# Performance work log

Measured on AMD Instinct MI355X. Metric: run time of the kernel, lower is better.

## Reference

```python
import jax, jax.numpy as jnp
import numpy as np

B, CIN, C, H, W = 8, 256, 128, 128, 128
BN_EPS = 1e-5
EPS = 1e-12


def _bn_params(k, c):
    k1, k2, k3, k4 = jax.random.split(k, 4)
    gamma = jax.random.uniform(k1, (c,), minval=0.5, maxval=1.5)
    beta = jax.random.normal(k2, (c,)) * 0.1
    mean = jax.random.normal(k3, (c,)) * 0.1
    var = jax.random.uniform(k4, (c,), minval=0.5, maxval=1.5)
    return gamma, beta, mean, var


def _xavier(k, cout, cin):
    lim = np.sqrt(6.0 / (cin + cout))
    return jax.random.uniform(k, (cout, cin), minval=-lim, maxval=lim)


def setup_inputs() -> dict:
    key = jax.random.key(0)
    ks = jax.random.split(key, 16)
    inp = {
        'target_task_feats': jax.random.normal(ks[0], (B, CIN, H, W), dtype=jnp.float32),
        'source_task_feats': jax.random.normal(ks[1], (B, CIN, H, W), dtype=jnp.float32),
        'q_w1': _xavier(ks[2], C, CIN), 'q_w2': _xavier(ks[3], C, C),
        'k_w1': _xavier(ks[4], C, CIN), 'k_w2': _xavier(ks[5], C, C),
        'v_w': _xavier(ks[6], C, CIN),
    }
    for name, kk, c in [('q1', ks[7], C), ('q2', ks[8], C), ('k1', ks[9], C), ('k2', ks[10], C), ('v', ks[11], C)]:
        g, b, m, v = _bn_params(kk, c)
        inp[f'{name}_g'], inp[f'{name}_b'], inp[f'{name}_m'], inp[f'{name}_v'] = g, b, m, v
    return inp


def _conv_bn(x, w, g, b, m, v):
    # 1x1 conv (no bias) + eval-mode BatchNorm, fused scale/shift
    y = jnp.einsum('bchw,oc->bohw', x, w)
    scale = (g / jnp.sqrt(v + BN_EPS))[None, :, None, None]
    shift = (b - m * g / jnp.sqrt(v + BN_EPS))[None, :, None, None]
    return y * scale + shift


def reference(target_task_feats, source_task_feats,
              q_w1, q_w2, k_w1, k_w2, v_w,
              q1_g, q1_b, q1_m, q1_v,
              q2_g, q2_b, q2_m, q2_v,
              k1_g, k1_b, k1_m, k1_v,
              k2_g, k2_b, k2_m, k2_v,
              v_g, v_b, v_m, v_v):
    b = target_task_feats.shape[0]
    # key / value from source
    k_h = jax.nn.relu(_conv_bn(source_task_feats, k_w1, k1_g, k1_b, k1_m, k1_v))
    key = jax.nn.softplus(_conv_bn(k_h, k_w2, k2_g, k2_b, k2_m, k2_v)).reshape(b, C, -1)  # [B,C,Ns]
    value = jax.nn.relu(_conv_bn(source_task_feats, v_w, v_g, v_b, v_m, v_v)).reshape(b, C, -1)  # [B,C,Ns]
    # query from target
    q_h = jax.nn.relu(_conv_bn(target_task_feats, q_w1, q1_g, q1_b, q1_m, q1_v))
    query = jax.nn.softplus(_conv_bn(q_h, q_w2, q2_g, q2_b, q2_m, q2_v)).reshape(b, C, -1)  # [B,C,Nt]
    # linear attention: KV^T then Q
    S = jnp.einsum('bcn,bdn->bcd', value, key)      # [B,C,C]
    Z = key.sum(axis=2)                              # [B,C]
    denom = jnp.einsum('bc,bcn->bn', Z, query)[:, None, :]  # [B,1,Nt]
    out = jnp.einsum('bcd,bdn->bcn', S, query) / jnp.maximum(denom, EPS)
    return out.reshape(b, C, H, W)
```

## Files before the change

### kernel.cpp

```cpp
#include <hip/hip_runtime.h>
#include <math.h>

typedef __attribute__((ext_vector_type(8))) short bf8v;
typedef __attribute__((ext_vector_type(4))) float f4v;

#define B_      8
#define CIN_    256
#define C_      128
#define NPIX_   16384
#define EPS_    1e-12f
#define BN_EPS_ 1e-5f

#define OFF_WK1  0u
#define OFF_WV   65536u
#define OFF_WQ1  131072u
#define OFF_WK2  196608u
#define OFF_WQ2  229376u
#define OFF_BIAS 262144u
#define OFF_S    264704u
#define OFF_Z    788992u
#define OFF_SBF  793088u
#define OFF_VAL  1055232u
#define OFF_KEY  34609664u

__device__ __forceinline__ unsigned short f2bf(float f) {
    unsigned u = __float_as_uint(f);
    unsigned r = u + 0x7fffu + ((u >> 16) & 1u);
    return (unsigned short)(r >> 16);
}
__device__ __forceinline__ float lo16(unsigned v){ return __uint_as_float(v << 16); }
__device__ __forceinline__ float hi16(unsigned v){ return __uint_as_float(v & 0xffff0000u); }
__device__ __forceinline__ float softplus_f(float x) {
    return fmaxf(x, 0.f) + __logf(1.f + __expf(-fabsf(x)));
}
__device__ __forceinline__ f4v MFMA(bf8v a, bf8v b, f4v c) {
    return __builtin_amdgcn_mfma_f32_16x16x32_bf16(a, b, c, 0, 0, 0);
}

struct PrepPtrs {
    const float* w[5];
    const float* g[5];
    const float* be[5];
    const float* mu[5];
    const float* va[5];
    unsigned short* wout[5];
    float* bout[5];
};

__global__ void prep_kernel(PrepPtrs p) {
    int idx = blockIdx.x * 256 + threadIdx.x;
    if (idx < 131072) {
        int conv, local, sh;
        if (idx < 32768)       { conv = 0; local = idx;          sh = 8; }
        else if (idx < 65536)  { conv = 1; local = idx - 32768;  sh = 8; }
        else if (idx < 98304)  { conv = 2; local = idx - 65536;  sh = 8; }
        else if (idx < 114688) { conv = 3; local = idx - 98304;  sh = 7; }
        else                   { conv = 4; local = idx - 114688; sh = 7; }
        int o = local >> sh;
        float scale = p.g[conv][o] * rsqrtf(p.va[conv][o] + BN_EPS_);
        p.wout[conv][local] = f2bf(p.w[conv][local] * scale);
    } else if (idx < 131712) {
        int j = idx - 131072;
        int conv = j >> 7;
        int o = j & 127;
        float scale = p.g[conv][o] * rsqrtf(p.va[conv][o] + BN_EPS_);
        p.bout[conv][o] = p.be[conv][o] - p.mu[conv][o] * scale;
    }
}

__global__ __launch_bounds__(256)
void srcKV(const float* __restrict__ src,
           const unsigned short* __restrict__ Wk1, const unsigned short* __restrict__ Wv,
           const unsigned short* __restrict__ Wk2, const float* __restrict__ bias,
           unsigned short* __restrict__ valg, unsigned short* __restrict__ keyg)
{
    __shared__ __align__(16) char smem[52224];
    unsigned short* xT = (unsigned short*)smem;
    unsigned short* hT = (unsigned short*)(smem + 33792);

    const int tid = threadIdx.x;
    const int L = tid & 63, w = tid >> 6;
    const int lr = L & 15, qd = L >> 4;
    const int b = blockIdx.y;
    const int gn0 = blockIdx.x * 64;
    const int m0 = w * 32;
    const int kbq = qd * 8;
    const float* bk1 = bias + 0;
    const float* bvp = bias + 128;
    const float* bk2 = bias + 384;

    #pragma unroll
    for (int s = 0; s < 4; s++) {
        int id = tid + s * 256;
        int n4 = (id & 15) * 4;
        int k0 = (id >> 4) * 4;
        float4 r[4];
        #pragma unroll
        for (int i = 0; i < 4; i++)
            r[i] = *(const float4*)(src + (size_t)(b * 256 + k0 + i) * NPIX_ + gn0 + n4);
        #pragma unroll
        for (int j = 0; j < 4; j++) {
            ushort4 t;
            t.x = f2bf(((const float*)&r[0])[j]);
            t.y = f2bf(((const float*)&r[1])[j]);
            t.z = f2bf(((const float*)&r[2])[j]);
            t.w = f2bf(((const float*)&r[3])[j]);
            *(ushort4*)(xT + (n4 + j) * 264 + k0) = t;
        }
    }
    __syncthreads();

    f4v zz = {0.f, 0.f, 0.f, 0.f};
    f4v hAcc[2][4], vAcc[2][4];
    #pragma unroll
    for (int mt = 0; mt < 2; mt++)
        #pragma unroll
        for (int nt = 0; nt < 4; nt++) { hAcc[mt][nt] = zz; vAcc[mt][nt] = zz; }
    #pragma unroll
    for (int ks = 0; ks < 8; ks++) {
        const int kb = ks * 32 + kbq;
        bf8v a1[2], a2[2], bx[4];
        #pragma unroll
        for (int mt = 0; mt < 2; mt++) {
            a1[mt] = *(const bf8v*)(Wk1 + (m0 + mt * 16 + lr) * 256 + kb);
            a2[mt] = *(const bf8v*)(Wv  + (m0 + mt * 16 + lr) * 256 + kb);
        }
        #pragma unroll
        for (int nt = 0; nt < 4; nt++)
            bx[nt] = *(const bf8v*)(xT + (nt * 16 + lr) * 264 + kb);
        #pragma unroll
        for (int mt = 0; mt < 2; mt++)
            #pragma unroll
            for (int nt = 0; nt < 4; nt++) {
                hAcc[mt][nt] = MFMA(a1[mt], bx[nt], hAcc[mt][nt]);
                vAcc[mt][nt] = MFMA(a2[mt], bx[nt], vAcc[mt][nt]);
            }
    }
    #pragma unroll
    for (int mt = 0; mt < 2; mt++) {
        const float4 b4 = *(const float4*)(bk1 + m0 + mt * 16 + qd * 4);
        #pragma unroll
        for (int nt = 0; nt < 4; nt++) {
            ushort4 t;
            t.x = f2bf(fmaxf(hAcc[mt][nt][0] + b4.x, 0.f));
            t.y = f2bf(fmaxf(hAcc[mt][nt][1] + b4.y, 0.f));
            t.z = f2bf(fmaxf(hAcc[mt][nt][2] + b4.z, 0.f));
            t.w = f2bf(fmaxf(hAcc[mt][nt][3] + b4.w, 0.f));
            *(ushort4*)(hT + (nt * 16 + lr) * 136 + m0 + mt * 16 + qd * 4) = t;
        }
    }
    __syncthreads();
    #pragma unroll
    for (int mt = 0; mt < 2; mt++) {
        const float4 b4 = *(const float4*)(bvp + m0 + mt * 16 + qd * 4);
        const float* bp = (const float*)&b4;
        #pragma unroll
        for (int nt = 0; nt < 4; nt++)
            #pragma unroll
            for (int r = 0; r < 4; r++)
                vAcc[mt][nt][r] = fmaxf(vAcc[mt][nt][r] + bp[r], 0.f);
    }

    f4v kAcc[2][4];
    #pragma unroll
    for (int mt = 0; mt < 2; mt++)
        #pragma unroll
        for (int nt = 0; nt < 4; nt++) kAcc[mt][nt] = zz;
    #pragma unroll
    for (int ks = 0; ks < 4; ks++) {
        const int kb = ks * 32 + kbq;
        bf8v a[2], bh[4];
        #pragma unroll
        for (int mt = 0; mt < 2; mt++)
            a[mt] = *(const bf8v*)(Wk2 + (m0 + mt * 16 + lr) * 128 + kb);
        #pragma unroll
        for (int nt = 0; nt < 4; nt++)
            bh[nt] = *(const bf8v*)(hT + (nt * 16 + lr) * 136 + kb);
        #pragma unroll
        for (int mt = 0; mt < 2; mt++)
            #pragma unroll
            for (int nt = 0; nt < 4; nt++)
                kAcc[mt][nt] = MFMA(a[mt], bh[nt], kAcc[mt][nt]);
    }
    __syncthreads();

    unsigned short* stgV = xT;
    unsigned short* stgK = hT;
    #pragma unroll
    for (int mt = 0; mt < 2; mt++) {
        const float4 b4 = *(const float4*)(bk2 + m0 + mt * 16 + qd * 4);
        const float* bp = (const float*)&b4;
        #pragma unroll
        for (int nt = 0; nt < 4; nt++)
            #pragma unroll
            for (int r = 0; r < 4; r++) {
                int m = m0 + mt * 16 + qd * 4 + r;
                stgV[m * 72 + nt * 16 + lr] = f2bf(vAcc[mt][nt][r]);
                stgK[m * 72 + nt * 16 + lr] = f2bf(softplus_f(kAcc[mt][nt][r] + bp[r]));
            }
    }
    __syncthreads();
    #pragma unroll
    for (int s = 0; s < 8; s++) {
        int id = tid + s * 256;
        int arr = id >> 10, rem = id & 1023;
        int c = rem >> 3, o = rem & 7;
        const unsigned short* sp = (arr ? stgK : stgV) + c * 72 + o * 8;
        uint4 d = *(const uint4*)sp;
        unsigned short* gp = (arr ? keyg : valg) + (size_t)(b * 128 + c) * NPIX_ + gn0 + o * 8;
        *(uint4*)gp = d;
    }
}

__global__ __launch_bounds__(256)
void skern(const unsigned short* __restrict__ valg, const unsigned short* __restrict__ keyg,
           float* __restrict__ Sbuf, float* __restrict__ Zbuf)
{
    __shared__ __align__(16) unsigned short vs[128 * 72];
    __shared__ __align__(16) unsigned short ks_[128 * 72];
    const int tid = threadIdx.x;
    const int L = tid & 63, w = tid >> 6;
    const int lr = L & 15, qd = L >> 4;
    const int b = blockIdx.x >> 5, ch = blockIdx.x & 31;
    const size_t nbase = (size_t)ch * 512;
    const int m0 = (w & 1) * 64, n0 = (w >> 1) * 64;

    f4v zz = {0.f, 0.f, 0.f, 0.f};
    f4v acc[4][4];
    #pragma unroll
    for (int mt = 0; mt < 4; mt++)
        #pragma unroll
        for (int nt = 0; nt < 4; nt++) acc[mt][nt] = zz;
    float zacc = 0.f;
    const int zc = tid >> 1, zh = tid & 1;

    for (int wd = 0; wd < 8; wd++) {
        const size_t nw = nbase + wd * 64;
        #pragma unroll
        for (int s = 0; s < 8; s++) {
            int id = tid + s * 256;
            int arr = id >> 10, rem = id & 1023;
            int c = rem >> 3, o = rem & 7;
            const unsigned short* g = (arr ? keyg : valg) + (size_t)(b * 128 + c) * NPIX_ + nw + o * 8;
            uint4 d = *(const uint4*)g;
            *(uint4*)((arr ? ks_ : vs) + c * 72 + o * 8) = d;
        }
        __syncthreads();
        #pragma unroll
        for (int kk = 0; kk < 2; kk++) {
            const int kb = kk * 32 + qd * 8;
            bf8v a[4], bb[4];
            #pragma unroll
            for (int mt = 0; mt < 4; mt++)
                a[mt] = *(const bf8v*)(vs + (m0 + mt * 16 + lr) * 72 + kb);
            #pragma unroll
            for (int nt = 0; nt < 4; nt++)
                bb[nt] = *(const bf8v*)(ks_ + (n0 + nt * 16 + lr) * 72 + kb);
            #pragma unroll
            for (int mt = 0; mt < 4; mt++)
                #pragma unroll
                for (int nt = 0; nt < 4; nt++)
                    acc[mt][nt] = MFMA(a[mt], bb[nt], acc[mt][nt]);
        }
        {
            const unsigned short* kr = ks_ + zc * 72 + zh * 32;
            #pragma unroll
            for (int p = 0; p < 4; p++) {
                uint4 t = *(const uint4*)(kr + p * 8);
                zacc += lo16(t.x) + hi16(t.x) + lo16(t.y) + hi16(t.y)
                      + lo16(t.z) + hi16(t.z) + lo16(t.w) + hi16(t.w);
            }
        }
        __syncthreads();
    }
    #pragma unroll
    for (int mt = 0; mt < 4; mt++)
        #pragma unroll
        for (int nt = 0; nt < 4; nt++)
            #pragma unroll
            for (int r = 0; r < 4; r++) {
                int m = m0 + mt * 16 + qd * 4 + r;
                int cN = n0 + nt * 16 + lr;
                atomicAdd(Sbuf + ((size_t)b * 128 + m) * 128 + cN, acc[mt][nt][r]);
            }
    atomicAdd(Zbuf + b * 128 + zc, zacc);
}

__global__ void cvts(const float* __restrict__ Sbuf, unsigned short* __restrict__ Sbf) {
    int i = blockIdx.x * 256 + threadIdx.x;
    if (i < 131072) Sbf[i] = f2bf(Sbuf[i]);
}

__global__ __launch_bounds__(256)
void tgtAttn(const float* __restrict__ tgt,
             const unsigned short* __restrict__ Wq1, const unsigned short* __restrict__ Wq2,
             const float* __restrict__ bias, const unsigned short* __restrict__ Sbf,
             const float* __restrict__ Zbuf, float* __restrict__ out)
{
    __shared__ __align__(16) char smem[51968];
    unsigned short* xT = (unsigned short*)smem;
    unsigned short* qT = (unsigned short*)(smem + 33792);
    float* dn  = (float*)(smem + 33792 + 17408);
    float* Zsh = dn + 64;

    const int tid = threadIdx.x;
    const int L = tid & 63, w = tid >> 6;
    const int lr = L & 15, qd = L >> 4;
    const int b = blockIdx.y;
    const int gn0 = blockIdx.x * 64;
    const int m0 = w * 32;
    const int kbq = qd * 8;
    const float* bq1 = bias + 256;
    const float* bq2 = bias + 512;

    if (tid < 128) Zsh[tid] = Zbuf[b * 128 + tid];
    #pragma unroll
    for (int s = 0; s < 4; s++) {
        int id = tid + s * 256;
        int n4 = (id & 15) * 4;
        int k0 = (id >> 4) * 4;
        float4 r[4];
        #pragma unroll
        for (int i = 0; i < 4; i++)
            r[i] = *(const float4*)(tgt + (size_t)(b * 256 + k0 + i) * NPIX_ + gn0 + n4);
        #pragma unroll
        for (int j = 0; j < 4; j++) {
            ushort4 t;
            t.x = f2bf(((const float*)&r[0])[j]);
            t.y = f2bf(((const float*)&r[1])[j]);
            t.z = f2bf(((const float*)&r[2])[j]);
            t.w = f2bf(((const float*)&r[3])[j]);
            *(ushort4*)(xT + (n4 + j) * 264 + k0) = t;
        }
    }
    __syncthreads();

    f4v zz = {0.f, 0.f, 0.f, 0.f};
    f4v acc1[2][4];
    #pragma unroll
    for (int mt = 0; mt < 2; mt++)
        #pragma unroll
        for (int nt = 0; nt < 4; nt++) acc1[mt][nt] = zz;
    #pragma unroll
    for (int ks = 0; ks < 8; ks++) {
        const int kb = ks * 32 + kbq;
        bf8v a[2], bx[4];
        #pragma unroll
        for (int mt = 0; mt < 2; mt++)
            a[mt] = *(const bf8v*)(Wq1 + (m0 + mt * 16 + lr) * 256 + kb);
        #pragma unroll
        for (int nt = 0; nt < 4; nt++)
            bx[nt] = *(const bf8v*)(xT + (nt * 16 + lr) * 264 + kb);
        #pragma unroll
        for (int mt = 0; mt < 2; mt++)
            #pragma unroll
            for (int nt = 0; nt < 4; nt++)
                acc1[mt][nt] = MFMA(a[mt], bx[nt], acc1[mt][nt]);
    }
    #pragma unroll
    for (int mt = 0; mt < 2; mt++) {
        const float4 b4 = *(const float4*)(bq1 + m0 + mt * 16 + qd * 4);
        #pragma unroll
        for (int nt = 0; nt < 4; nt++) {
            ushort4 t;
            t.x = f2bf(fmaxf(acc1[mt][nt][0] + b4.x, 0.f));
            t.y = f2bf(fmaxf(acc1[mt][nt][1] + b4.y, 0.f));
            t.z = f2bf(fmaxf(acc1[mt][nt][2] + b4.z, 0.f));
            t.w = f2bf(fmaxf(acc1[mt][nt][3] + b4.w, 0.f));
            *(ushort4*)(qT + (nt * 16 + lr) * 136 + m0 + mt * 16 + qd * 4) = t;
        }
    }
    __syncthreads();

    f4v acc2[2][4];
    #pragma unroll
    for (int mt = 0; mt < 2; mt++)
        #pragma unroll
        for (int nt = 0; nt < 4; nt++) acc2[mt][nt] = zz;
    #pragma unroll
    for (int ks = 0; ks < 4; ks++) {
        const int kb = ks * 32 + kbq;
        bf8v a[2], bh[4];
        #pragma unroll
        for (int mt = 0; mt < 2; mt++)
            a[mt] = *(const bf8v*)(Wq2 + (m0 + mt * 16 + lr) * 128 + kb);
        #pragma unroll
        for (int nt = 0; nt < 4; nt++)
            bh[nt] = *(const bf8v*)(qT + (nt * 16 + lr) * 136 + kb);
        #pragma unroll
        for (int mt = 0; mt < 2; mt++)
            #pragma unroll
            for (int nt = 0; nt < 4; nt++)
                acc2[mt][nt] = MFMA(a[mt], bh[nt], acc2[mt][nt]);
    }
    __syncthreads();
    #pragma unroll
    for (int mt = 0; mt < 2; mt++) {
        const float4 b4 = *(const float4*)(bq2 + m0 + mt * 16 + qd * 4);
        const float* bp = (const float*)&b4;
        #pragma unroll
        for (int nt = 0; nt < 4; nt++) {
            ushort4 t;
            t.x = f2bf(softplus_f(acc2[mt][nt][0] + bp[0]));
            t.y = f2bf(softplus_f(acc2[mt][nt][1] + bp[1]));
            t.z = f2bf(softplus_f(acc2[mt][nt][2] + bp[2]));
            t.w = f2bf(softplus_f(acc2[mt][nt][3] + bp[3]));
            *(ushort4*)(qT + (nt * 16 + lr) * 136 + m0 + mt * 16 + qd * 4) = t;
        }
    }
    __syncthreads();

    if (tid < 64) {
        const unsigned short* qr = qT + tid * 136;
        float s = 0.f;
        #pragma unroll
        for (int d = 0; d < 128; d += 8) {
            uint4 t = *(const uint4*)(qr + d);
            s = fmaf(Zsh[d + 0], lo16(t.x), s);
            s = fmaf(Zsh[d + 1], hi16(t.x), s);
            s = fmaf(Zsh[d + 2], lo16(t.y), s);
            s = fmaf(Zsh[d + 3], hi16(t.y), s);
            s = fmaf(Zsh[d + 4], lo16(t.z), s);
            s = fmaf(Zsh[d + 5], hi16(t.z), s);
            s = fmaf(Zsh[d + 6], lo16(t.w), s);
            s = fmaf(Zsh[d + 7], hi16(t.w), s);
        }
        dn[tid] = fmaxf(s, EPS_);
    }

    f4v oacc[2][4];
    #pragma unroll
    for (int mt = 0; mt < 2; mt++)
        #pragma unroll
        for (int nt = 0; nt < 4; nt++) oacc[mt][nt] = zz;
    #pragma unroll
    for (int ks = 0; ks < 4; ks++) {
        const int kb = ks * 32 + kbq;
        bf8v a[2], bq[4];
        #pragma unroll
        for (int mt = 0; mt < 2; mt++)
            a[mt] = *(const bf8v*)(Sbf + (size_t)b * 16384 + (m0 + mt * 16 + lr) * 128 + kb);
        #pragma unroll
        for (int nt = 0; nt < 4; nt++)
            bq[nt] = *(const bf8v*)(qT + (nt * 16 + lr) * 136 + kb);
        #pragma unroll
        for (int mt = 0; mt < 2; mt++)
            #pragma unroll
            for (int nt = 0; nt < 4; nt++)
                oacc[mt][nt] = MFMA(a[mt], bq[nt], oacc[mt][nt]);
    }
    __syncthreads();

    float inv[4];
    #pragma unroll
    for (int nt = 0; nt < 4; nt++) inv[nt] = 1.f / dn[nt * 16 + lr];
    #pragma unroll
    for (int mt = 0; mt < 2; mt++)
        #pragma unroll
        for (int nt = 0; nt < 4; nt++)
            #pragma unroll
            for (int r = 0; r < 4; r++) {
                int m = m0 + mt * 16 + qd * 4 + r;
                out[(size_t)(b * 128 + m) * NPIX_ + gn0 + nt * 16 + lr] = oacc[mt][nt][r] * inv[nt];
            }
}

extern "C" void kernel_launch(void* const* d_in, const int* in_sizes, int n_in,
                              void* d_out, int out_size, void* d_ws, size_t ws_size,
                              hipStream_t stream)
{
    const float* tgt = (const float*)d_in[0];
    const float* src = (const float*)d_in[1];
    char* ws = (char*)d_ws;
    unsigned short* Wk1 = (unsigned short*)(ws + OFF_WK1);
    unsigned short* Wv  = (unsigned short*)(ws + OFF_WV);
    unsigned short* Wq1 = (unsigned short*)(ws + OFF_WQ1);
    unsigned short* Wk2 = (unsigned short*)(ws + OFF_WK2);
    unsigned short* Wq2 = (unsigned short*)(ws + OFF_WQ2);
    float* bias = (float*)(ws + OFF_BIAS);
    float* Sbuf = (float*)(ws + OFF_S);
    float* Zbuf = (float*)(ws + OFF_Z);
    unsigned short* Sbf = (unsigned short*)(ws + OFF_SBF);
    unsigned short* valg = (unsigned short*)(ws + OFF_VAL);
    unsigned short* keyg = (unsigned short*)(ws + OFF_KEY);

    PrepPtrs p;
    p.w[0] = (const float*)d_in[4];
    p.w[1] = (const float*)d_in[6];
    p.w[2] = (const float*)d_in[2];
    p.w[3] = (const float*)d_in[5];
    p.w[4] = (const float*)d_in[3];
    const int gbase[5] = {15, 23, 7, 19, 11};
    for (int c = 0; c < 5; c++) {
        p.g[c]  = (const float*)d_in[gbase[c]];
        p.be[c] = (const float*)d_in[gbase[c] + 1];
        p.mu[c] = (const float*)d_in[gbase[c] + 2];
        p.va[c] = (const float*)d_in[gbase[c] + 3];
    }
    p.wout[0] = Wk1; p.wout[1] = Wv; p.wout[2] = Wq1; p.wout[3] = Wk2; p.wout[4] = Wq2;
    p.bout[0] = bias; p.bout[1] = bias + 128; p.bout[2] = bias + 256;
    p.bout[3] = bias + 384; p.bout[4] = bias + 512;

    hipMemsetAsync(ws + OFF_S, 0, 524288 + 4096, stream);
    hipLaunchKernelGGL(prep_kernel, dim3(515), dim3(256), 0, stream, p);
    hipLaunchKernelGGL(srcKV, dim3(256, 8), dim3(256), 0, stream,
                       src, Wk1, Wv, Wk2, bias, valg, keyg);
    hipLaunchKernelGGL(skern, dim3(256), dim3(256), 0, stream, valg, keyg, Sbuf, Zbuf);
    hipLaunchKernelGGL(cvts, dim3(512), dim3(256), 0, stream, Sbuf, Sbf);
    hipLaunchKernelGGL(tgtAttn, dim3(256, 8), dim3(256), 0, stream,
                       tgt, Wq1, Wq2, bias, Sbf, Zbuf, (float*)d_out);
}
```

Before: 453.9 us.

## Use 512-thread blocks with register prefetch of next tile and swizzled LDS

srcKV and tgtAttn move to 512-thread blocks that each handle two 64-pixel tiles. The next tile's fp32 input is loaded into registers while the current tile is computed, and the transposed LDS layout gets an XOR swizzle in place of padding. skern doubles its grid, splitting the pixel range into smaller chunks, and double-buffers its global loads through registers. The aim is to hide global memory latency and raise occupancy, at the cost of more registers per thread and extra barriers.

New measurement: 636.3 us. 1.4x slower.

```diff
diff --git a/kernel.cpp b/kernel.cpp
--- a/kernel.cpp
+++ b/kernel.cpp
@@ -10,6 +10,7 @@
 #define NPIX_   16384
 #define EPS_    1e-12f
 #define BN_EPS_ 1e-5f
+#define TPB2_   2
 
 #define OFF_WK1  0u
 #define OFF_WV   65536u
@@ -68,151 +69,158 @@
     }
 }
 
-__global__ __launch_bounds__(256)
+
+__global__ __launch_bounds__(512, 4)
 void srcKV(const float* __restrict__ src,
            const unsigned short* __restrict__ Wk1, const unsigned short* __restrict__ Wv,
            const unsigned short* __restrict__ Wk2, const float* __restrict__ bias,
            unsigned short* __restrict__ valg, unsigned short* __restrict__ keyg)
 {
-    __shared__ __align__(16) char smem[52224];
-    unsigned short* xT = (unsigned short*)smem;
-    unsigned short* hT = (unsigned short*)(smem + 33792);
+    __shared__ __align__(16) char smem[50176];
+    unsigned short* xT   = (unsigned short*)smem;
+    unsigned short* hT   = (unsigned short*)(smem + 32768);
+    unsigned short* stgV = (unsigned short*)smem;
+    unsigned short* stgK = (unsigned short*)(smem + 18432);
 
     const int tid = threadIdx.x;
     const int L = tid & 63, w = tid >> 6;
     const int lr = L & 15, qd = L >> 4;
     const int b = blockIdx.y;
-    const int gn0 = blockIdx.x * 64;
-    const int m0 = w * 32;
+    const int m0 = w * 16;
     const int kbq = qd * 8;
-    const float* bk1 = bias + 0;
+    const float* bk1 = bias;
     const float* bvp = bias + 128;
     const float* bk2 = bias + 384;
-
-    #pragma unroll
-    for (int s = 0; s < 4; s++) {
-        int id = tid + s * 256;
-        int n4 = (id & 15) * 4;
-        int k0 = (id >> 4) * 4;
-        float4 r[4];
-        #pragma unroll
-        for (int i = 0; i < 4; i++)
-            r[i] = *(const float4*)(src + (size_t)(b * 256 + k0 + i) * NPIX_ + gn0 + n4);
-        #pragma unroll
-        for (int j = 0; j < 4; j++) {
-            ushort4 t;
-            t.x = f2bf(((const float*)&r[0])[j]);
-            t.y = f2bf(((const float*)&r[1])[j]);
-            t.z = f2bf(((const float*)&r[2])[j]);
-            t.w = f2bf(((const float*)&r[3])[j]);
-            *(ushort4*)(xT + (n4 + j) * 264 + k0) = t;
-        }
-    }
-    __syncthreads();
-
-    f4v zz = {0.f, 0.f, 0.f, 0.f};
-    f4v hAcc[2][4], vAcc[2][4];
-    #pragma unroll
-    for (int mt = 0; mt < 2; mt++)
-        #pragma unroll
-        for (int nt = 0; nt < 4; nt++) { hAcc[mt][nt] = zz; vAcc[mt][nt] = zz; }
-    #pragma unroll
-    for (int ks = 0; ks < 8; ks++) {
-        const int kb = ks * 32 + kbq;
-        bf8v a1[2], a2[2], bx[4];
-        #pragma unroll
-        for (int mt = 0; mt < 2; mt++) {
-            a1[mt] = *(const bf8v*)(Wk1 + (m0 + mt * 16 + lr) * 256 + kb);
-            a2[mt] = *(const bf8v*)(Wv  + (m0 + mt * 16 + lr) * 256 + kb);
-        }
-        #pragma unroll
-        for (int nt = 0; nt < 4; nt++)
-            bx[nt] = *(const bf8v*)(xT + (nt * 16 + lr) * 264 + kb);
-        #pragma unroll
-        for (int mt = 0; mt < 2; mt++)
-            #pragma unroll
-            for (int nt = 0; nt < 4; nt++) {
-                hAcc[mt][nt] = MFMA(a1[mt], bx[nt], hAcc[mt][nt]);
-                vAcc[mt][nt] = MFMA(a2[mt], bx[nt], vAcc[mt][nt]);
-            }
-    }
-    #pragma unroll
-    for (int mt = 0; mt < 2; mt++) {
-        const float4 b4 = *(const float4*)(bk1 + m0 + mt * 16 + qd * 4);
-        #pragma unroll
-        for (int nt = 0; nt < 4; nt++) {
-            ushort4 t;
-            t.x = f2bf(fmaxf(hAcc[mt][nt][0] + b4.x, 0.f));
-            t.y = f2bf(fmaxf(hAcc[mt][nt][1] + b4.y, 0.f));
-            t.z = f2bf(fmaxf(hAcc[mt][nt][2] + b4.z, 0.f));
-            t.w = f2bf(fmaxf(hAcc[mt][nt][3] + b4.w, 0.f));
-            *(ushort4*)(hT + (nt * 16 + lr) * 136 + m0 + mt * 16 + qd * 4) = t;
-        }
-    }
-    __syncthreads();
-    #pragma unroll
-    for (int mt = 0; mt < 2; mt++) {
-        const float4 b4 = *(const float4*)(bvp + m0 + mt * 16 + qd * 4);
-        const float* bp = (const float*)&b4;
-        #pragma unroll
-        for (int nt = 0; nt < 4; nt++)
-            #pragma unroll
-            for (int r = 0; r < 4; r++)
-                vAcc[mt][nt][r] = fmaxf(vAcc[mt][nt][r] + bp[r], 0.f);
-    }
-
-    f4v kAcc[2][4];
-    #pragma unroll
-    for (int mt = 0; mt < 2; mt++)
-        #pragma unroll
-        for (int nt = 0; nt < 4; nt++) kAcc[mt][nt] = zz;
-    #pragma unroll
-    for (int ks = 0; ks < 4; ks++) {
-        const int kb = ks * 32 + kbq;
-        bf8v a[2], bh[4];
-        #pragma unroll
-        for (int mt = 0; mt < 2; mt++)
-            a[mt] = *(const bf8v*)(Wk2 + (m0 + mt * 16 + lr) * 128 + kb);
-        #pragma unroll
-        for (int nt = 0; nt < 4; nt++)
-            bh[nt] = *(const bf8v*)(hT + (nt * 16 + lr) * 136 + kb);
-        #pragma unroll
-        for (int mt = 0; mt < 2; mt++)
-            #pragma unroll
-            for (int nt = 0; nt < 4; nt++)
-                kAcc[mt][nt] = MFMA(a[mt], bh[nt], kAcc[mt][nt]);
-    }
-    __syncthreads();
-
-    unsigned short* stgV = xT;
-    unsigned short* stgK = hT;
-    #pragma unroll
-    for (int mt = 0; mt < 2; mt++) {
-        const float4 b4 = *(const float4*)(bk2 + m0 + mt * 16 + qd * 4);
-        const float* bp = (const float*)&b4;
-        #pragma unroll
-        for (int nt = 0; nt < 4; nt++)
-            #pragma unroll
-            for (int r = 0; r < 4; r++) {
-                int m = m0 + mt * 16 + qd * 4 + r;
-                stgV[m * 72 + nt * 16 + lr] = f2bf(vAcc[mt][nt][r]);
-                stgK[m * 72 + nt * 16 + lr] = f2bf(softplus_f(kAcc[mt][nt][r] + bp[r]));
-            }
-    }
-    __syncthreads();
-    #pragma unroll
-    for (int s = 0; s < 8; s++) {
-        int id = tid + s * 256;
-        int arr = id >> 10, rem = id & 1023;
-        int c = rem >> 3, o = rem & 7;
-        const unsigned short* sp = (arr ? stgK : stgV) + c * 72 + o * 8;
-        uint4 d = *(const uint4*)sp;
-        unsigned short* gp = (arr ? keyg : valg) + (size_t)(b * 128 + c) * NPIX_ + gn0 + o * 8;
-        *(uint4*)gp = d;
-    }
-}
-
-__global__ __launch_bounds__(256)
+    const int pn4 = (tid & 15) * 4;
+
+    float4 pf[8];
+    int tile = blockIdx.x * TPB2_;
+    {
+        const int gn0 = tile * 64;
+        #pragma unroll
+        for (int s = 0; s < 2; s++) {
+            const int k0 = ((tid >> 4) + s * 32) * 4;
+            const float* gp = src + (size_t)(b * 256 + k0) * NPIX_ + gn0 + pn4;
+            #pragma unroll
+            for (int i = 0; i < 4; i++)
+                pf[s * 4 + i] = *(const float4*)(gp + (size_t)i * NPIX_);
+        }
+    }
+
+    for (int tt = 0; tt < TPB2_; tt++, tile++) {
+        const int gn0 = tile * 64;
+        if (tt) __syncthreads();
+        #pragma unroll
+        for (int s = 0; s < 2; s++) {
+            const int k0 = ((tid >> 4) + s * 32) * 4;
+            const int c = k0 >> 3, h4 = k0 & 4;
+            #pragma unroll
+            for (int j = 0; j < 4; j++) {
+                const int row = pn4 + j;
+                ushort4 t;
+                t.x = f2bf(((const float*)&pf[s*4+0])[j]);
+                t.y = f2bf(((const float*)&pf[s*4+1])[j]);
+                t.z = f2bf(((const float*)&pf[s*4+2])[j]);
+                t.w = f2bf(((const float*)&pf[s*4+3])[j]);
+                *(ushort4*)(xT + row * 256 + (((c ^ (row & 31)) << 3) | h4)) = t;
+            }
+        }
+        __syncthreads();
+        if (tt + 1 < TPB2_) {
+            const int gn1 = (tile + 1) * 64;
+            #pragma unroll
+            for (int s = 0; s < 2; s++) {
+                const int k0 = ((tid >> 4) + s * 32) * 4;
+                const float* gp = src + (size_t)(b * 256 + k0) * NPIX_ + gn1 + pn4;
+                #pragma unroll
+                for (int i = 0; i < 4; i++)
+                    pf[s * 4 + i] = *(const float4*)(gp + (size_t)i * NPIX_);
+            }
+        }
+
+        f4v zz = {0.f, 0.f, 0.f, 0.f};
+        f4v hA[4] = {zz, zz, zz, zz}, vA[4] = {zz, zz, zz, zz};
+        #pragma unroll
+        for (int ks = 0; ks < 8; ks++) {
+            const int kb = ks * 32 + kbq;
+            const int cch = kb >> 3;
+            bf8v a1 = *(const bf8v*)(Wk1 + (m0 + lr) * 256 + kb);
+            bf8v a2 = *(const bf8v*)(Wv  + (m0 + lr) * 256 + kb);
+            bf8v bx[4];
+            #pragma unroll
+            for (int nt = 0; nt < 4; nt++) {
+                const int row = nt * 16 + lr;
+                bx[nt] = *(const bf8v*)(xT + row * 256 + ((cch ^ (row & 31)) << 3));
+            }
+            #pragma unroll
+            for (int nt = 0; nt < 4; nt++) {
+                hA[nt] = MFMA(a1, bx[nt], hA[nt]);
+                vA[nt] = MFMA(a2, bx[nt], vA[nt]);
+            }
+        }
+        {
+            const float4 b4 = *(const float4*)(bk1 + m0 + qd * 4);
+            #pragma unroll
+            for (int nt = 0; nt < 4; nt++) {
+                ushort4 t;
+                t.x = f2bf(fmaxf(hA[nt][0] + b4.x, 0.f));
+                t.y = f2bf(fmaxf(hA[nt][1] + b4.y, 0.f));
+                t.z = f2bf(fmaxf(hA[nt][2] + b4.z, 0.f));
+                t.w = f2bf(fmaxf(hA[nt][3] + b4.w, 0.f));
+                *(ushort4*)(hT + (nt * 16 + lr) * 136 + m0 + qd * 4) = t;
+            }
+            const float4 bv4 = *(const float4*)(bvp + m0 + qd * 4);
+            const float* bp = (const float*)&bv4;
+            #pragma unroll
+            for (int nt = 0; nt < 4; nt++)
+                #pragma unroll
+                for (int r = 0; r < 4; r++)
+                    vA[nt][r] = fmaxf(vA[nt][r] + bp[r], 0.f);
+        }
+        __syncthreads();
+
+        f4v kA[4] = {zz, zz, zz, zz};
+        #pragma unroll
+        for (int ks = 0; ks < 4; ks++) {
+            const int kb = ks * 32 + kbq;
+            bf8v a = *(const bf8v*)(Wk2 + (m0 + lr) * 128 + kb);
+            bf8v bh[4];
+            #pragma unroll
+            for (int nt = 0; nt < 4; nt++)
+                bh[nt] = *(const bf8v*)(hT + (nt * 16 + lr) * 136 + kb);
+            #pragma unroll
+            for (int nt = 0; nt < 4; nt++)
+                kA[nt] = MFMA(a, bh[nt], kA[nt]);
+        }
+        __syncthreads();
+
+        {
+            const float4 bK4 = *(const float4*)(bk2 + m0 + qd * 4);
+            const float* bp = (const float*)&bK4;
+            #pragma unroll
+            for (int nt = 0; nt < 4; nt++) {
+                const int n = nt * 16 + lr;
+                #pragma unroll
+                for (int r = 0; r < 4; r++) {
+                    const int m = m0 + qd * 4 + r;
+                    stgV[m * 72 + n] = f2bf(vA[nt][r]);
+                    stgK[m * 72 + n] = f2bf(softplus_f(kA[nt][r] + bp[r]));
+                }
+            }
+        }
+        __syncthreads();
+        #pragma unroll
+        for (int s = 0; s < 4; s++) {
+            const int id2 = tid + s * 512;
+            const int arr = id2 >> 10, rem = id2 & 1023;
+            const int c = rem >> 3, o = rem & 7;
+            uint4 d = *(const uint4*)((arr ? stgK : stgV) + c * 72 + o * 8);
+            *(uint4*)((arr ? keyg : valg) + (size_t)(b * 128 + c) * NPIX_ + gn0 + o * 8) = d;
+        }
+    }
+}
+
+__global__ __launch_bounds__(256, 3)
 void skern(const unsigned short* __restrict__ valg, const unsigned short* __restrict__ keyg,
            float* __restrict__ Sbuf, float* __restrict__ Zbuf)
 {
@@ -221,9 +229,12 @@
     const int tid = threadIdx.x;
     const int L = tid & 63, w = tid >> 6;
     const int lr = L & 15, qd = L >> 4;
-    const int b = blockIdx.x >> 5, ch = blockIdx.x & 31;
-    const size_t nbase = (size_t)ch * 512;
+    const int b = blockIdx.x >> 6, ch = blockIdx.x & 63;
+    const size_t nbase = (size_t)ch * 256;
     const int m0 = (w & 1) * 64, n0 = (w >> 1) * 64;
+    const int sarr = tid >> 7 ? 1 : 0;
+
+    const int sc[8] = {0,0,0,0,0,0,0,0}; (void)sc; (void)sarr;
 
     f4v zz = {0.f, 0.f, 0.f, 0.f};
     f4v acc[4][4];
@@ -234,18 +245,36 @@
     float zacc = 0.f;
     const int zc = tid >> 1, zh = tid & 1;
 
-    for (int wd = 0; wd < 8; wd++) {
-        const size_t nw = nbase + wd * 64;
+    uint4 pf[8];
+    {
         #pragma unroll
         for (int s = 0; s < 8; s++) {
-            int id = tid + s * 256;
-            int arr = id >> 10, rem = id & 1023;
-            int c = rem >> 3, o = rem & 7;
-            const unsigned short* g = (arr ? keyg : valg) + (size_t)(b * 128 + c) * NPIX_ + nw + o * 8;
-            uint4 d = *(const uint4*)g;
-            *(uint4*)((arr ? ks_ : vs) + c * 72 + o * 8) = d;
-        }
-        __syncthreads();
+            const int id = tid + s * 256;
+            const int arr = id >> 10, rem = id & 1023;
+            const int c = rem >> 3, o = rem & 7;
+            pf[s] = *(const uint4*)((arr ? keyg : valg) + (size_t)(b * 128 + c) * NPIX_ + nbase + o * 8);
+        }
+    }
+
+    for (int wd = 0; wd < 4; wd++) {
+        #pragma unroll
+        for (int s = 0; s < 8; s++) {
+            const int id = tid + s * 256;
+            const int arr = id >> 10, rem = id & 1023;
+            const int c = rem >> 3, o = rem & 7;
+            *(uint4*)((arr ? ks_ : vs) + c * 72 + o * 8) = pf[s];
+        }
+        __syncthreads();
+        if (wd < 3) {
+            const size_t nw = nbase + (wd + 1) * 64;
+            #pragma unroll
+            for (int s = 0; s < 8; s++) {
+                const int id = tid + s * 256;
+                const int arr = id >> 10, rem = id & 1023;
+                const int c = rem >> 3, o = rem & 7;
+                pf[s] = *(const uint4*)((arr ? keyg : valg) + (size_t)(b * 128 + c) * NPIX_ + nw + o * 8);
+            }
+        }
         #pragma unroll
         for (int kk = 0; kk < 2; kk++) {
             const int kb = kk * 32 + qd * 8;
@@ -291,178 +320,178 @@
     if (i < 131072) Sbf[i] = f2bf(Sbuf[i]);
 }
 
-__global__ __launch_bounds__(256)
+__global__ __launch_bounds__(512, 4)
 void tgtAttn(const float* __restrict__ tgt,
              const unsigned short* __restrict__ Wq1, const unsigned short* __restrict__ Wq2,
              const float* __restrict__ bias, const unsigned short* __restrict__ Sbf,
              const float* __restrict__ Zbuf, float* __restrict__ out)
 {
-    __shared__ __align__(16) char smem[51968];
+    __shared__ __align__(16) char smem[50944];
     unsigned short* xT = (unsigned short*)smem;
-    unsigned short* qT = (unsigned short*)(smem + 33792);
-    float* dn  = (float*)(smem + 33792 + 17408);
-    float* Zsh = dn + 64;
+    unsigned short* hT = (unsigned short*)(smem + 32768);
+    float* dn  = (float*)(smem + 50176);
+    float* Zsh = (float*)(smem + 50432);
 
     const int tid = threadIdx.x;
     const int L = tid & 63, w = tid >> 6;
     const int lr = L & 15, qd = L >> 4;
     const int b = blockIdx.y;
-    const int gn0 = blockIdx.x * 64;
-    const int m0 = w * 32;
+    const int m0 = w * 16;
     const int kbq = qd * 8;
     const float* bq1 = bias + 256;
     const float* bq2 = bias + 512;
+    const int pn4 = (tid & 15) * 4;
 
     if (tid < 128) Zsh[tid] = Zbuf[b * 128 + tid];
-    #pragma unroll
-    for (int s = 0; s < 4; s++) {
-        int id = tid + s * 256;
-        int n4 = (id & 15) * 4;
-        int k0 = (id >> 4) * 4;
-        float4 r[4];
-        #pragma unroll
-        for (int i = 0; i < 4; i++)
-            r[i] = *(const float4*)(tgt + (size_t)(b * 256 + k0 + i) * NPIX_ + gn0 + n4);
-        #pragma unroll
-        for (int j = 0; j < 4; j++) {
-            ushort4 t;
-            t.x = f2bf(((const float*)&r[0])[j]);
-            t.y = f2bf(((const float*)&r[1])[j]);
-            t.z = f2bf(((const float*)&r[2])[j]);
-            t.w = f2bf(((const float*)&r[3])[j]);
-            *(ushort4*)(xT + (n4 + j) * 264 + k0) = t;
-        }
-    }
-    __syncthreads();
-
-    f4v zz = {0.f, 0.f, 0.f, 0.f};
-    f4v acc1[2][4];
-    #pragma unroll
-    for (int mt = 0; mt < 2; mt++)
-        #pragma unroll
-        for (int nt = 0; nt < 4; nt++) acc1[mt][nt] = zz;
-    #pragma unroll
-    for (int ks = 0; ks < 8; ks++) {
-        const int kb = ks * 32 + kbq;
-        bf8v a[2], bx[4];
-        #pragma unroll
-        for (int mt = 0; mt < 2; mt++)
-            a[mt] = *(const bf8v*)(Wq1 + (m0 + mt * 16 + lr) * 256 + kb);
+
+    float4 pf[8];
+    int tile = blockIdx.x * TPB2_;
+    {
+        const int gn0 = tile * 64;
+        #pragma unroll
+        for (int s = 0; s < 2; s++) {
+            const int k0 = ((tid >> 4) + s * 32) * 4;
+            const float* gp = tgt + (size_t)(b * 256 + k0) * NPIX_ + gn0 + pn4;
+            #pragma unroll
+            for (int i = 0; i < 4; i++)
+                pf[s * 4 + i] = *(const float4*)(gp + (size_t)i * NPIX_);
+        }
+    }
+
+    for (int tt = 0; tt < TPB2_; tt++, tile++) {
+        const int gn0 = tile * 64;
+        if (tt) __syncthreads();
+        #pragma unroll
+        for (int s = 0; s < 2; s++) {
+            const int k0 = ((tid >> 4) + s * 32) * 4;
+            const int c = k0 >> 3, h4 = k0 & 4;
+            #pragma unroll
+            for (int j = 0; j < 4; j++) {
+                const int row = pn4 + j;
+                ushort4 t;
+                t.x = f2bf(((const float*)&pf[s*4+0])[j]);
+                t.y = f2bf(((const float*)&pf[s*4+1])[j]);
+                t.z = f2bf(((const float*)&pf[s*4+2])[j]);
+                t.w = f2bf(((const float*)&pf[s*4+3])[j]);
+                *(ushort4*)(xT + row * 256 + (((c ^ (row & 31)) << 3) | h4)) = t;
+            }
+        }
+        __syncthreads();
+        if (tt + 1 < TPB2_) {
+            const int gn1 = (tile + 1) * 64;
+            #pragma unroll
+            for (int s = 0; s < 2; s++) {
+                const int k0 = ((tid >> 4) + s * 32) * 4;
+                const float* gp = tgt + (size_t)(b * 256 + k0) * NPIX_ + gn1 + pn4;
+                #pragma unroll
+                for (int i = 0; i < 4; i++)
+                    pf[s * 4 + i] = *(const float4*)(gp + (size_t)i * NPIX_);
+            }
+        }
+
+        f4v zz = {0.f, 0.f, 0.f, 0.f};
+        f4v a1c[4] = {zz, zz, zz, zz};
+        #pragma unroll
+        for (int ks = 0; ks < 8; ks++) {
+            const int kb = ks * 32 + kbq;
+            const int cch = kb >> 3;
+            bf8v a = *(const bf8v*)(Wq1 + (m0 + lr) * 256 + kb);
+            bf8v bx[4];
+            #pragma unroll
+            for (int nt = 0; nt < 4; nt++) {
+                const int row = nt * 16 + lr;
+                bx[nt] = *(const bf8v*)(xT + row * 256 + ((cch ^ (row & 31)) << 3));
+            }
+            #pragma unroll
+            for (int nt = 0; nt < 4; nt++)
+                a1c[nt] = MFMA(a, bx[nt], a1c[nt]);
+        }
+        {
+            const float4 b4 = *(const float4*)(bq1 + m0 + qd * 4);
+            #pragma unroll
+            for (int nt = 0; nt < 4; nt++) {
+                ushort4 t;
+                t.x = f2bf(fmaxf(a1c[nt][0] + b4.x, 0.f));
+                t.y = f2bf(fmaxf(a1c[nt][1] + b4.y, 0.f));
+                t.z = f2bf(fmaxf(a1c[nt][2] + b4.z, 0.f));
+                t.w = f2bf(fmaxf(a1c[nt][3] + b4.w, 0.f));
+                *(ushort4*)(hT + (nt * 16 + lr) * 136 + m0 + qd * 4) = t;
+            }
+        }
+        __syncthreads();
+
+        f4v a2c[4] = {zz, zz, zz, zz};
+        #pragma unroll
+        for (int ks = 0; ks < 4; ks++) {
+            const int kb = ks * 32 + kbq;
+            bf8v a = *(const bf8v*)(Wq2 + (m0 + lr) * 128 + kb);
+            bf8v bh[4];
+            #pragma unroll
+            for (int nt = 0; nt < 4; nt++)
+                bh[nt] = *(const bf8v*)(hT + (nt * 16 + lr) * 136 + kb);
+            #pragma unroll
+            for (int nt = 0; nt < 4; nt++)
+                a2c[nt] = MFMA(a, bh[nt], a2c[nt]);
+        }
+        __syncthreads();
+        {
+            const float4 b4 = *(const float4*)(bq2 + m0 + qd * 4);
+            const float* bp = (const float*)&b4;
+            #pragma unroll
+            for (int nt = 0; nt < 4; nt++) {
+                ushort4 t;
+                t.x = f2bf(softplus_f(a2c[nt][0] + bp[0]));
+                t.y = f2bf(softplus_f(a2c[nt][1] + bp[1]));
+                t.z = f2bf(softplus_f(a2c[nt][2] + bp[2]));
+                t.w = f2bf(softplus_f(a2c[nt][3] + bp[3]));
+                *(ushort4*)(hT + (nt * 16 + lr) * 136 + m0 + qd * 4) = t;
+            }
+        }
+        __syncthreads();
+
+        if (tid < 64) {
+            const unsigned short* qr = hT + tid * 136;
+            float s = 0.f;
+            #pragma unroll
+            for (int d = 0; d < 128; d += 8) {
+                uint4 t = *(const uint4*)(qr + d);
+                s = fmaf(Zsh[d + 0], lo16(t.x), s);
+                s = fmaf(Zsh[d + 1], hi16(t.x), s);
+                s = fmaf(Zsh[d + 2], lo16(t.y), s);
+                s = fmaf(Zsh[d + 3], hi16(t.y), s);
+                s = fmaf(Zsh[d + 4], lo16(t.z), s);
+                s = fmaf(Zsh[d + 5], hi16(t.z), s);
+                s = fmaf(Zsh[d + 6], lo16(t.w), s);
+                s = fmaf(Zsh[d + 7], hi16(t.w), s);
+            }
+            dn[tid] = fmaxf(s, EPS_);
+        }
+        f4v oacc[4] = {zz, zz, zz, zz};
+        #pragma unroll
+        for (int ks = 0; ks < 4; ks++) {
+            const int kb = ks * 32 + kbq;
+            bf8v a = *(const bf8v*)(Sbf + (size_t)b * 16384 + (m0 + lr) * 128 + kb);
+            bf8v bq[4];
+            #pragma unroll
+            for (int nt = 0; nt < 4; nt++)
+                bq[nt] = *(const bf8v*)(hT + (nt * 16 + lr) * 136 + kb);
+            #pragma unroll
+            for (int nt = 0; nt < 4; nt++)
+                oacc[nt] = MFMA(a, bq[nt], oacc[nt]);
+        }
+        __syncthreads();
+
+        float inv[4];
+        #pragma unroll
+        for (int nt = 0; nt < 4; nt++) inv[nt] = 1.f / dn[nt * 16 + lr];
         #pragma unroll
         for (int nt = 0; nt < 4; nt++)
-            bx[nt] = *(const bf8v*)(xT + (nt * 16 + lr) * 264 + kb);
-        #pragma unroll
-        for (int mt = 0; mt < 2; mt++)
-            #pragma unroll
-            for (int nt = 0; nt < 4; nt++)
-                acc1[mt][nt] = MFMA(a[mt], bx[nt], acc1[mt][nt]);
-    }
-    #pragma unroll
-    for (int mt = 0; mt < 2; mt++) {
-        const float4 b4 = *(const float4*)(bq1 + m0 + mt * 16 + qd * 4);
-        #pragma unroll
-        for (int nt = 0; nt < 4; nt++) {
-            ushort4 t;
-            t.x = f2bf(fmaxf(acc1[mt][nt][0] + b4.x, 0.f));
-            t.y = f2bf(fmaxf(acc1[mt][nt][1] + b4.y, 0.f));
-            t.z = f2bf(fmaxf(acc1[mt][nt][2] + b4.z, 0.f));
-            t.w = f2bf(fmaxf(acc1[mt][nt][3] + b4.w, 0.f));
-            *(ushort4*)(qT + (nt * 16 + lr) * 136 + m0 + mt * 16 + qd * 4) = t;
-        }
-    }
-    __syncthreads();
-
-    f4v acc2[2][4];
-    #pragma unroll
-    for (int mt = 0; mt < 2; mt++)
-        #pragma unroll
-        for (int nt = 0; nt < 4; nt++) acc2[mt][nt] = zz;
-    #pragma unroll
-    for (int ks = 0; ks < 4; ks++) {
-        const int kb = ks * 32 + kbq;
-        bf8v a[2], bh[4];
-        #pragma unroll
-        for (int mt = 0; mt < 2; mt++)
-            a[mt] = *(const bf8v*)(Wq2 + (m0 + mt * 16 + lr) * 128 + kb);
-        #pragma unroll
-        for (int nt = 0; nt < 4; nt++)
-            bh[nt] = *(const bf8v*)(qT + (nt * 16 + lr) * 136 + kb);
-        #pragma unroll
-        for (int mt = 0; mt < 2; mt++)
-            #pragma unroll
-            for (int nt = 0; nt < 4; nt++)
-                acc2[mt][nt] = MFMA(a[mt], bh[nt], acc2[mt][nt]);
-    }
-    __syncthreads();
-    #pragma unroll
-    for (int mt = 0; mt < 2; mt++) {
-        const float4 b4 = *(const float4*)(bq2 + m0 + mt * 16 + qd * 4);
-        const float* bp = (const float*)&b4;
-        #pragma unroll
-        for (int nt = 0; nt < 4; nt++) {
-            ushort4 t;
-            t.x = f2bf(softplus_f(acc2[mt][nt][0] + bp[0]));
-            t.y = f2bf(softplus_f(acc2[mt][nt][1] + bp[1]));
-            t.z = f2bf(softplus_f(acc2[mt][nt][2] + bp[2]));
-            t.w = f2bf(softplus_f(acc2[mt][nt][3] + bp[3]));
-            *(ushort4*)(qT + (nt * 16 + lr) * 136 + m0 + mt * 16 + qd * 4) = t;
-        }
-    }
-    __syncthreads();
-
-    if (tid < 64) {
-        const unsigned short* qr = qT + tid * 136;
-        float s = 0.f;
-        #pragma unroll
-        for (int d = 0; d < 128; d += 8) {
-            uint4 t = *(const uint4*)(qr + d);
-            s = fmaf(Zsh[d + 0], lo16(t.x), s);
-            s = fmaf(Zsh[d + 1], hi16(t.x), s);
-            s = fmaf(Zsh[d + 2], lo16(t.y), s);
-            s = fmaf(Zsh[d + 3], hi16(t.y), s);
-            s = fmaf(Zsh[d + 4], lo16(t.z), s);
-            s = fmaf(Zsh[d + 5], hi16(t.z), s);
-            s = fmaf(Zsh[d + 6], lo16(t.w), s);
-            s = fmaf(Zsh[d + 7], hi16(t.w), s);
-        }
-        dn[tid] = fmaxf(s, EPS_);
-    }
-
-    f4v oacc[2][4];
-    #pragma unroll
-    for (int mt = 0; mt < 2; mt++)
-        #pragma unroll
-        for (int nt = 0; nt < 4; nt++) oacc[mt][nt] = zz;
-    #pragma unroll
-    for (int ks = 0; ks < 4; ks++) {
-        const int kb = ks * 32 + kbq;
-        bf8v a[2], bq[4];
-        #pragma unroll
-        for (int mt = 0; mt < 2; mt++)
-            a[mt] = *(const bf8v*)(Sbf + (size_t)b * 16384 + (m0 + mt * 16 + lr) * 128 + kb);
-        #pragma unroll
-        for (int nt = 0; nt < 4; nt++)
-            bq[nt] = *(const bf8v*)(qT + (nt * 16 + lr) * 136 + kb);
-        #pragma unroll
-        for (int mt = 0; mt < 2; mt++)
-            #pragma unroll
-            for (int nt = 0; nt < 4; nt++)
-                oacc[mt][nt] = MFMA(a[mt], bq[nt], oacc[mt][nt]);
-    }
-    __syncthreads();
-
-    float inv[4];
-    #pragma unroll
-    for (int nt = 0; nt < 4; nt++) inv[nt] = 1.f / dn[nt * 16 + lr];
-    #pragma unroll
-    for (int mt = 0; mt < 2; mt++)
-        #pragma unroll
-        for (int nt = 0; nt < 4; nt++)
             #pragma unroll
             for (int r = 0; r < 4; r++) {
-                int m = m0 + mt * 16 + qd * 4 + r;
-                out[(size_t)(b * 128 + m) * NPIX_ + gn0 + nt * 16 + lr] = oacc[mt][nt][r] * inv[nt];
-            }
+                const int m = m0 + qd * 4 + r;
+                out[(size_t)(b * 128 + m) * NPIX_ + gn0 + nt * 16 + lr] = oacc[nt][r] * inv[nt];
+            }
+    }
 }
 
 extern "C" void kernel_launch(void* const* d_in, const int* in_sizes, int n_in,
@@ -503,10 +532,10 @@
 
     hipMemsetAsync(ws + OFF_S, 0, 524288 + 4096, stream);
     hipLaunchKernelGGL(prep_kernel, dim3(515), dim3(256), 0, stream, p);
-    hipLaunchKernelGGL(srcKV, dim3(256, 8), dim3(256), 0, stream,
+    hipLaunchKernelGGL(srcKV, dim3(128, 8), dim3(512), 0, stream,
                        src, Wk1, Wv, Wk2, bias, valg, keyg);
-    hipLaunchKernelGGL(skern, dim3(256), dim3(256), 0, stream, valg, keyg, Sbuf, Zbuf);
+    hipLaunchKernelGGL(skern, dim3(512), dim3(256), 0, stream, valg, keyg, Sbuf, Zbuf);
     hipLaunchKernelGGL(cvts, dim3(512), dim3(256), 0, stream, Sbuf, Sbf);
-    hipLaunchKernelGGL(tgtAttn, dim3(256, 8), dim3(256), 0, stream,
+    hipLaunchKernelGGL(tgtAttn, dim3(128, 8), dim3(512), 0, stream,
                        tgt, Wq1, Wq2, bias, Sbf, Zbuf, (float*)d_out);
 }
```
